# Kernel optimization log

Measured on AMD Instinct MI355X. Metric: run time of the kernel, lower is better.

## Reference

```python
import jax, jax.numpy as jnp
import numpy as np
from math import sqrt

L, H, D, HD, F, V, P = 8, 16, 1024, 64, 4096, 32000, 2048
B, S = 2, 2048
EPS = 1e-5


def _ln(x, g, b):
    m = jnp.mean(x, axis=-1, keepdims=True)
    v = jnp.mean((x - m) ** 2, axis=-1, keepdims=True)
    return (x - m) * jax.lax.rsqrt(v + EPS) * g + b


def setup_inputs() -> dict:
    key = jax.random.key(0)
    ks = jax.random.split(key, 12)
    w = 0.02
    return {
        'input_ids': jax.random.randint(ks[0], (B, S), 0, V),
        'tok_emb': jax.random.normal(ks[1], (V, D), jnp.float32) * w,
        'pos_emb': jax.random.normal(ks[2], (P, D), jnp.float32) * w,
        'emb_g': jnp.ones((D,), jnp.float32),
        'emb_b': jnp.zeros((D,), jnp.float32),
        'ln1_g': jnp.ones((L, D), jnp.float32),
        'ln1_b': jnp.zeros((L, D), jnp.float32),
        'ln2_g': jnp.ones((L, D), jnp.float32),
        'ln2_b': jnp.zeros((L, D), jnp.float32),
        'Wq': jax.random.normal(ks[3], (L, H, D, HD), jnp.float32) * w,
        'bq': jnp.zeros((L, H, HD), jnp.float32),
        'Wk': jax.random.normal(ks[4], (L, H, D, HD), jnp.float32) * w,
        'bk': jnp.zeros((L, H, HD), jnp.float32),
        'Wv': jax.random.normal(ks[5], (L, H, D, HD), jnp.float32) * w,
        'bv': jnp.zeros((L, H, HD), jnp.float32),
        'Wo': jax.random.normal(ks[6], (L, D, D), jnp.float32) * w,
        'bo': jnp.zeros((L, D), jnp.float32),
        'W1': jax.random.normal(ks[7], (L, D, F), jnp.float32) * w,
        'b1': jnp.zeros((L, F), jnp.float32),
        'W2': jax.random.normal(ks[8], (L, F, D), jnp.float32) * w,
        'b2': jnp.zeros((L, D), jnp.float32),
    }


def _encoder(input_ids, tok_emb, pos_emb, emb_g, emb_b, ln1_g, ln1_b, ln2_g,
             ln2_b, Wq, bq, Wk, bk, Wv, bv, Wo, bo, W1, b1, W2, b2):
    seq = input_ids.shape[-1]
    x = tok_emb[input_ids] + pos_emb[:seq][None, :, :]  # [B,S,D]
    x = _ln(x, emb_g, emb_b)  # dropout = identity (eval)

    scale = 1.0 / sqrt(HD)

    def layer(x, p):
        (g1, b1_, g2, b2_, wq, bq_, wk, bk_, wv, bv_, wo, bo_, w1, bb1, w2, bb2) = p
        h = _ln(x, g1, b1_)
        q = jnp.einsum('bsd,hdk->bhsk', h, wq) + bq_[:, None, :]
        k = jnp.einsum('bsd,hdk->bhsk', h, wk) + bk_[:, None, :]
        v = jnp.einsum('bsd,hdk->bhsk', h, wv) + bv_[:, None, :]
        scores = jnp.einsum('bhsk,bhtk->bhst', q, k) * scale
        w = jax.nn.softmax(scores, axis=-1)
        av = jnp.einsum('bhst,bhtk->bhsk', w, v)  # [B,H,S,hd]
        av = jnp.transpose(av, (0, 2, 1, 3)).reshape(x.shape[0], x.shape[1], D)
        x = x + jnp.einsum('bsd,de->bse', av, wo) + bo_
        h2 = _ln(x, g2, b2_)
        f = jax.nn.gelu(jnp.einsum('bsd,df->bsf', h2, w1) + bb1, approximate=False)
        x = x + jnp.einsum('bsf,fd->bsd', f, w2) + bb2
        return x, None

    xs = (ln1_g, ln1_b, ln2_g, ln2_b, Wq, bq, Wk, bk, Wv, bv, Wo, bo, W1, b1, W2, b2)
    x, _ = jax.lax.scan(layer, x, xs)
    return x


def reference(input_ids, tok_emb, pos_emb, emb_g, emb_b, ln1_g, ln1_b, ln2_g,
              ln2_b, Wq, bq, Wk, bk, Wv, bv, Wo, bo, W1, b1, W2, b2):
    return _encoder(input_ids, tok_emb, pos_emb, emb_g, emb_b, ln1_g, ln1_b,
                    ln2_g, ln2_b, Wq, bq, Wk, bk, Wv, bv, Wo, bo, W1, b1, W2, b2)
```

## Files before the change

kernel.cpp:

```cpp
#include <hip/hip_runtime.h>
#include <hip/hip_bf16.h>

#define L_ 8
#define H_ 16
#define D_ 1024
#define HD_ 64
#define F_ 4096
#define B_ 2
#define S_ 2048
#define NTOK (B_*S_)

typedef unsigned short u16;
typedef __bf16 bf16x8 __attribute__((ext_vector_type(8)));
typedef float f32x4 __attribute__((ext_vector_type(4)));

__device__ __forceinline__ u16 f2b(float f){ union{float f; unsigned u;} c; c.f = f; unsigned u = c.u; return (u16)((u + 0x7fffu + ((u>>16)&1u)) >> 16); }
__device__ __forceinline__ u16 f2b_fast(float f){ union{float f; unsigned u;} c; c.f = f; return (u16)((c.u + 0x8000u) >> 16); }
__device__ __forceinline__ float b2f(u16 x){ union{unsigned u; float f;} c; c.u = ((unsigned)x)<<16; return c.f; }

__device__ __forceinline__ void gload16(const u16* g, u16* l){
  __builtin_amdgcn_global_load_lds(
      (const __attribute__((address_space(1))) void*)g,
      (__attribute__((address_space(3))) void*)l,
      16 , 0 , 0 );
}

__device__ __forceinline__ void lds_fence(){
  asm volatile("s_waitcnt lgkmcnt(0)" ::: "memory");
  __builtin_amdgcn_sched_barrier(0);
}

#define WAITV_BAR(n) do { \
  asm volatile("s_waitcnt vmcnt(%0)" :: "i"(n) : "memory"); \
  __builtin_amdgcn_sched_barrier(0); \
  __builtin_amdgcn_s_barrier(); \
} while(0)

__device__ __forceinline__ void blk_reduce2(float& a, float& b, float* sm){
  for (int off=32; off>0; off>>=1){ a += __shfl_down(a,off); b += __shfl_down(b,off); }
  int w = threadIdx.x>>6, ln = threadIdx.x&63;
  if (ln==0){ sm[w]=a; sm[4+w]=b; }
  __syncthreads();
  a = sm[0]+sm[1]+sm[2]+sm[3];
  b = sm[4]+sm[5]+sm[6]+sm[7];
}

__global__ __launch_bounds__(256) void embed_ln(const int* __restrict__ ids,
    const float* __restrict__ tok, const float* __restrict__ pos,
    const float* __restrict__ g, const float* __restrict__ bb,
    float* __restrict__ x)
{
  __shared__ float sm[8];
  int row = blockIdx.x;
  int s   = row % S_;
  int id  = ids[row];
  int d0  = threadIdx.x*4;
  float4 t4 = *(const float4*)(tok + (size_t)id*D_ + d0);
  float4 p4 = *(const float4*)(pos + (size_t)s *D_ + d0);
  float4 v; v.x=t4.x+p4.x; v.y=t4.y+p4.y; v.z=t4.z+p4.z; v.w=t4.w+p4.w;
  float sum = (v.x+v.y)+(v.z+v.w);
  float sq  = v.x*v.x+v.y*v.y+v.z*v.z+v.w*v.w;
  blk_reduce2(sum, sq, sm);
  float mean = sum * (1.0f/D_);
  float var  = sq  * (1.0f/D_) - mean*mean;
  float inv  = rsqrtf(var + 1e-5f);
  float4 g4 = *(const float4*)(g + d0);
  float4 b4 = *(const float4*)(bb + d0);
  float4 o; o.x=(v.x-mean)*inv*g4.x+b4.x; o.y=(v.y-mean)*inv*g4.y+b4.y;
            o.z=(v.z-mean)*inv*g4.z+b4.z; o.w=(v.w-mean)*inv*g4.w+b4.w;
  *(float4*)(x + (size_t)row*D_ + d0) = o;
}

__global__ __launch_bounds__(256) void ln_f32_bf16(const float* __restrict__ x,
    const float* __restrict__ g, const float* __restrict__ bb, u16* __restrict__ out)
{
  __shared__ float sm[8];
  int row = blockIdx.x;
  int d0  = threadIdx.x*4;
  float4 v = *(const float4*)(x + (size_t)row*D_ + d0);
  float sum = (v.x+v.y)+(v.z+v.w);
  float sq  = v.x*v.x+v.y*v.y+v.z*v.z+v.w*v.w;
  blk_reduce2(sum, sq, sm);
  float mean = sum * (1.0f/D_);
  float var  = sq  * (1.0f/D_) - mean*mean;
  float inv  = rsqrtf(var + 1e-5f);
  float4 g4 = *(const float4*)(g + d0);
  float4 b4 = *(const float4*)(bb + d0);
  uint2 w;
  w.x = (unsigned)f2b((v.x-mean)*inv*g4.x+b4.x) | ((unsigned)f2b((v.y-mean)*inv*g4.y+b4.y)<<16);
  w.y = (unsigned)f2b((v.z-mean)*inv*g4.z+b4.z) | ((unsigned)f2b((v.w-mean)*inv*g4.w+b4.w)<<16);
  *(uint2*)(out + (size_t)row*D_ + d0) = w;
}

__global__ __launch_bounds__(256) void transpose_w(const float* __restrict__ src,
    u16* __restrict__ dst, int R, int C)
{
  __shared__ u16 tile[64*64];
  int c0 = blockIdx.x*64, r0 = blockIdx.y*64;
  int t = threadIdx.x;
  #pragma unroll
  for (int i=0;i<2;i++){
    int idx = t + i*256;
    int row = idx>>3, c8 = idx&7;
    const float* p = src + (size_t)(r0+row)*C + c0 + c8*8;
    float4 a = *(const float4*)p;
    float4 b = *(const float4*)(p+4);
    u16 tmp[8];
    tmp[0]=f2b(a.x); tmp[1]=f2b(a.y); tmp[2]=f2b(a.z); tmp[3]=f2b(a.w);
    tmp[4]=f2b(b.x); tmp[5]=f2b(b.y); tmp[6]=f2b(b.z); tmp[7]=f2b(b.w);
    int sw = (row&7) ^ ((row>>3)&7);
    *(uint4*)(&tile[row*64 + ((c8 ^ sw)<<3)]) = *(uint4*)tmp;
  }
  __syncthreads();
  #pragma unroll
  for (int i=0;i<2;i++){
    int idx = t + i*256;
    int oc = idx>>3, tc = idx&7;
    u16 tmp[8];
    #pragma unroll
    for (int j=0;j<8;j++){
      int rr = tc*8 + j;
      int sw = (rr&7) ^ ((rr>>3)&7);
      tmp[j] = tile[rr*64 + ((((oc>>3) ^ sw)<<3) | (oc&7))];
    }
    *(uint4*)(dst + (size_t)(c0+oc)*R + r0 + tc*8) = *(uint4*)tmp;
  }
}

__global__ __launch_bounds__(256) void qkv_repack(const float* __restrict__ Wq,
    const float* __restrict__ Wk, const float* __restrict__ Wv,
    u16* __restrict__ dst, int layer)
{
  __shared__ u16 tile[64*64];
  int z = blockIdx.y; int which = z >> 4, h = z & 15;
  const float* W = (which==0) ? Wq : (which==1) ? Wk : Wv;
  const float* src = W + ((size_t)(layer*H_ + h))*D_*HD_;
  int r0 = blockIdx.x*64;
  int t = threadIdx.x;
  #pragma unroll
  for (int i=0;i<2;i++){
    int idx = t + i*256;
    int row = idx>>3, c8 = idx&7;
    const float* p = src + (size_t)(r0+row)*HD_ + c8*8;
    float4 a = *(const float4*)p;
    float4 b = *(const float4*)(p+4);
    u16 tmp[8];
    tmp[0]=f2b(a.x); tmp[1]=f2b(a.y); tmp[2]=f2b(a.z); tmp[3]=f2b(a.w);
    tmp[4]=f2b(b.x); tmp[5]=f2b(b.y); tmp[6]=f2b(b.z); tmp[7]=f2b(b.w);
    int sw = (row&7) ^ ((row>>3)&7);
    *(uint4*)(&tile[row*64 + ((c8 ^ sw)<<3)]) = *(uint4*)tmp;
  }
  __syncthreads();
  #pragma unroll
  for (int i=0;i<2;i++){
    int idx = t + i*256;
    int oc = idx>>3, tc = idx&7;
    u16 tmp[8];
    #pragma unroll
    for (int j=0;j<8;j++){
      int rr = tc*8 + j;
      int sw = (rr&7) ^ ((rr>>3)&7);
      tmp[j] = tile[rr*64 + ((((oc>>3) ^ sw)<<3) | (oc&7))];
    }
    *(uint4*)(dst + (size_t)(which*1024 + h*64 + oc)*D_ + r0 + tc*8) = *(uint4*)tmp;
  }
}

__global__ __launch_bounds__(256) void v_transpose(const u16* __restrict__ qkv, u16* __restrict__ vT)
{
  __shared__ u16 tile[64*64];
  const int tt = blockIdx.x;
  const int bh = blockIdx.y;
  const int b = bh>>4, h = bh&15;
  const int t = threadIdx.x;
  const u16* src = qkv + (size_t)(b*S_ + tt*64)*3072 + 2048 + h*64;
  #pragma unroll
  for (int i=0;i<2;i++){
    int idx = t + i*256;
    int tl = idx>>3, hc = idx&7;
    uint4 v = *(const uint4*)(src + (size_t)tl*3072 + hc*8);
    int sw = (tl&7) ^ ((tl>>3)&7);
    *(uint4*)(&tile[tl*64 + ((hc ^ sw)<<3)]) = v;
  }
  __syncthreads();
  u16* dst = vT + ((size_t)bh*64)*S_ + tt*64;
  #pragma unroll
  for (int i=0;i<2;i++){
    int idx = t + i*256;
    int hd = idx>>3, tc = idx&7;
    u16 tmp[8];
    #pragma unroll
    for (int j=0;j<8;j++){
      int tk = tc*8 + j;
      int sw = (tk&7) ^ ((tk>>3)&7);
      tmp[j] = tile[tk*64 + ((((hd>>3) ^ sw)<<3) | (hd&7))];
    }
    *(uint4*)(dst + (size_t)hd*S_ + tc*8) = *(uint4*)tmp;
  }
}

__device__ __forceinline__ void epi_store(float v0,float v1,float v2,float v3,
    float* xres, u16* obf, size_t idx, int epi)
{
  if (epi==1){
    float4 t = *(float4*)(xres + idx);
    t.x += v0; t.y += v1; t.z += v2; t.w += v3;
    *(float4*)(xres + idx) = t;
  } else {
    if (epi==2){
      #define GELU_T(v) { float t2=(v)*(v); float u=(v)*fmaf(t2,0.044715f,1.0f); \
                          float e=exp2f(u*-2.3022082f); (v)=(v)*__builtin_amdgcn_rcpf(1.0f+e); }
      GELU_T(v0); GELU_T(v1); GELU_T(v2); GELU_T(v3);
      #undef GELU_T
    }
    uint2 w;
    w.x = (unsigned)f2b_fast(v0) | ((unsigned)f2b_fast(v1) << 16);
    w.y = (unsigned)f2b_fast(v2) | ((unsigned)f2b_fast(v3) << 16);
    *(uint2*)(obf + idx) = w;
  }
}

__global__ __launch_bounds__(256) void gemm_64x128(
    const u16* __restrict__ A, const u16* __restrict__ Bt,
    const float* __restrict__ bias0, float* __restrict__ xres,
    int M, int N, int K)
{
  __shared__ u16 As[64*64];
  __shared__ u16 Bs[128*64];
  const int tid = threadIdx.x;
  const int nbx = gridDim.x;
  const int nwg = nbx * gridDim.y;
  int bid = blockIdx.x + nbx*blockIdx.y;
  int nid = (bid & 7)*(nwg >> 3) + (bid >> 3);
  const int bm = (nid % nbx) * 64;
  const int bn = (nid / nbx) * 128;
  const int wv = tid>>6, ln = tid&63;
  const int wr = wv>>1, wc = wv&1;
  const int l15 = ln&15, lhi = ln>>4;
  const int l8 = ln>>3;
  const int c8s = (ln&7) ^ l8;
  f32x4 acc[2][4];
  const f32x4 zero4 = {0.f,0.f,0.f,0.f};
  #pragma unroll
  for (int i=0;i<2;i++)
    #pragma unroll
    for (int j=0;j<4;j++) acc[i][j] = zero4;

  for (int k0 = 0; k0 < K; k0 += 64) {
    #pragma unroll
    for (int i=0;i<2;i++){
      int row = wv*16 + i*8 + l8;
      gload16(A + (size_t)(bm+row)*K + k0 + c8s*8, &As[(wv*16 + i*8)*64]);
    }
    #pragma unroll
    for (int i=0;i<4;i++){
      int row = wv*32 + i*8 + l8;
      gload16(Bt + (size_t)(bn+row)*K + k0 + c8s*8, &Bs[(wv*32 + i*8)*64]);
    }
    __syncthreads();
    #pragma unroll
    for (int ks=0; ks<2; ks++){
      bf16x8 af[2], bfr[4];
      #pragma unroll
      for (int i=0;i<2;i++){
        int ra = wr*32 + i*16 + l15;
        af[i]  = *(const bf16x8*)(&As[ra*64 + (((ks*4+lhi) ^ (ra&7))<<3)]);
      }
      #pragma unroll
      for (int j=0;j<4;j++){
        int rb = wc*64 + j*16 + l15;
        bfr[j] = *(const bf16x8*)(&Bs[rb*64 + (((ks*4+lhi) ^ (rb&7))<<3)]);
      }
      #pragma unroll
      for (int i=0;i<2;i++)
        #pragma unroll
        for (int j=0;j<4;j++)
          acc[i][j] = __builtin_amdgcn_mfma_f32_16x16x32_bf16(bfr[j], af[i], acc[i][j], 0,0,0);
    }
    __syncthreads();
  }

  #pragma unroll
  for (int j=0;j<4;j++){
    int col0 = bn + wc*64 + j*16 + lhi*4;
    float4 bv4 = *(const float4*)(bias0 + col0);
    #pragma unroll
    for (int i=0;i<2;i++){
      int row = bm + wr*32 + i*16 + l15;
      size_t idx = (size_t)row*N + col0;
      float4 t = *(float4*)(xres + idx);
      t.x += acc[i][j][0] + bv4.x;
      t.y += acc[i][j][1] + bv4.y;
      t.z += acc[i][j][2] + bv4.z;
      t.w += acc[i][j][3] + bv4.w;
      *(float4*)(xres + idx) = t;
    }
  }
}

__global__ __launch_bounds__(512,2) void gemm256(
    const u16* __restrict__ A, const u16* __restrict__ Bt,
    const float* __restrict__ bias0, const float* __restrict__ bias1, const float* __restrict__ bias2,
    float* __restrict__ xres, u16* __restrict__ obf,
    int M, int N, int K, int epi)
{
  __shared__ u16 As[2][256*64];
  __shared__ u16 Bs[2][256*64];
  const int tid = threadIdx.x;
  const int nbx = gridDim.x;
  const int nwg = nbx * gridDim.y;
  int bid = blockIdx.x + nbx*blockIdx.y;
  int nid = (bid & 7)*(nwg >> 3) + (bid >> 3);
  const int bm = (nid % nbx) * 256;
  const int bn = (nid / nbx) * 256;
  const int wv = tid>>6, ln = tid&63;
  const int wm = wv>>2, wn = wv&3;
  const int l15 = ln&15, lhi = ln>>4;
  const int l8 = ln>>3;
  const int c8s = (ln&7) ^ l8;

  f32x4 acc[2][2][4][2];
  const f32x4 zero4 = {0.f,0.f,0.f,0.f};
  #pragma unroll
  for (int a=0;a<2;a++)
    #pragma unroll
    for (int b=0;b<2;b++)
      #pragma unroll
      for (int i=0;i<4;i++)
        #pragma unroll
        for (int j=0;j<2;j++) acc[a][b][i][j] = zero4;

  const u16* aB0 = A  + (size_t)(bm + wv*16 + l8)*K + c8s*8;
  const u16* bB0 = Bt + (size_t)(bn + wv*16 + l8)*K + c8s*8;

  #define ISSUE(c, kt) do {                                                  \
    const u16* aB = aB0 + (size_t)(kt)*64;                                   \
    const u16* bB = bB0 + (size_t)(kt)*64;                                   \
    gload16(aB,                 &As[c][(wv*16      )*64]);                   \
    gload16(aB + (size_t)8*K,   &As[c][(wv*16 +   8)*64]);                   \
    gload16(bB,                 &Bs[c][(wv*16      )*64]);                   \
    gload16(bB + (size_t)8*K,   &Bs[c][(wv*16 +   8)*64]);                   \
    gload16(bB + (size_t)128*K, &Bs[c][(128 + wv*16    )*64]);               \
    gload16(bB + (size_t)136*K, &Bs[c][(128 + wv*16 + 8)*64]);               \
    gload16(aB + (size_t)128*K, &As[c][(128 + wv*16    )*64]);               \
    gload16(aB + (size_t)136*K, &As[c][(128 + wv*16 + 8)*64]);               \
  } while(0)

  #define READ_B(c) do {                                                     \
    _Pragma("unroll")                                                        \
    for (int qc=0;qc<2;qc++)                                                 \
      _Pragma("unroll")                                                      \
      for (int j=0;j<2;j++){                                                 \
        int rb = qc*128 + wn*32 + j*16 + l15;                                \
        _Pragma("unroll")                                                    \
        for (int ks=0;ks<2;ks++)                                             \
          bfr[qc][j][ks] = *(const bf16x8*)(&Bs[c][rb*64 + (((ks*4+lhi) ^ (rb&7))<<3)]); \
      }                                                                      \
  } while(0)

  #define READ_A(c, qr) do {                                                 \
    _Pragma("unroll")                                                        \
    for (int i=0;i<4;i++){                                                   \
      int ra = (qr)*128 + wm*64 + i*16 + l15;                                \
      _Pragma("unroll")                                                      \
      for (int ks=0;ks<2;ks++)                                               \
        af[i][ks] = *(const bf16x8*)(&As[c][ra*64 + (((ks*4+lhi) ^ (ra&7))<<3)]); \
    }                                                                        \
  } while(0)

  #define MFMA_Q(qr) do {                                                    \
    __builtin_amdgcn_s_setprio(1);                                           \
    _Pragma("unroll")                                                        \
    for (int ks=0;ks<2;ks++)                                                 \
      _Pragma("unroll")                                                      \
      for (int i=0;i<4;i++)                                                  \
        _Pragma("unroll")                                                    \
        for (int qc=0;qc<2;qc++)                                             \
          _Pragma("unroll")                                                  \
          for (int j=0;j<2;j++)                                              \
            acc[qr][qc][i][j] = __builtin_amdgcn_mfma_f32_16x16x32_bf16(     \
                bfr[qc][j][ks], af[i][ks], acc[qr][qc][i][j], 0,0,0);        \
    __builtin_amdgcn_s_setprio(0);                                           \
  } while(0)

  const int nt = K >> 6;
  ISSUE(0, 0);
  WAITV_BAR(2);
  for (int t=0; t<nt-1; ++t){
    int c = t&1;
    ISSUE(c^1, t+1);
    bf16x8 bfr[2][2][2], af[4][2];
    READ_B(c);
    READ_A(c, 0);
    MFMA_Q(0);
    WAITV_BAR(8);
    READ_A(c, 1);
    MFMA_Q(1);
    WAITV_BAR(2);
  }
  {
    int c = (nt-1)&1;
    bf16x8 bfr[2][2][2], af[4][2];
    READ_B(c);
    READ_A(c, 0);
    MFMA_Q(0);
    WAITV_BAR(0);
    READ_A(c, 1);
    MFMA_Q(1);
  }
  #undef ISSUE
  #undef READ_B
  #undef READ_A
  #undef MFMA_Q

  #pragma unroll
  for (int qc=0; qc<2; qc++)
    #pragma unroll
    for (int j=0;j<2;j++){
      int col0 = bn + qc*128 + wn*32 + j*16 + lhi*4;
      float4 bv4;
      if (bias1){
        const float* bp = (col0 < 1024) ? (bias0 + col0)
                        : (col0 < 2048) ? (bias1 + col0 - 1024)
                                        : (bias2 + col0 - 2048);
        bv4 = *(const float4*)bp;
      } else {
        bv4 = *(const float4*)(bias0 + col0);
      }
      #pragma unroll
      for (int qr=0; qr<2; qr++)
        #pragma unroll
        for (int i=0;i<4;i++){
          int row = bm + qr*128 + wm*64 + i*16 + l15;
          epi_store(acc[qr][qc][i][j][0]+bv4.x, acc[qr][qc][i][j][1]+bv4.y,
                    acc[qr][qc][i][j][2]+bv4.z, acc[qr][qc][i][j][3]+bv4.w,
                    xres, obf, (size_t)row*N + col0, epi);
        }
    }
}

__global__ __launch_bounds__(256) void attn_fwd(const u16* __restrict__ qkv,
    const u16* __restrict__ vT, u16* __restrict__ att)
{
  __shared__ u16 Ks[2][64*64];
  __shared__ u16 Vs[2][64*64];
  __shared__ u16 Ps[4][2][16*64];
  const int tid = threadIdx.x, wv = tid>>6, ln = tid&63, l15 = ln&15, lhi = ln>>4;
  const int l8 = ln>>3;
  const int cs = (ln&7) ^ l8;
  int bid = blockIdx.x + 16*(blockIdx.y + 16*blockIdx.z);
  int nid = (bid & 7)*64 + (bid >> 3);
  const int qt = nid & 15, h = (nid >> 4) & 15, b = nid >> 8;
  const u16* qg = qkv + (size_t)b*S_*3072 + h*64;
  const u16* kg = qg + 1024;
  const u16* vtg = vT + ((size_t)(b*16 + h)*64)*S_;

  bf16x8 qfA[2], qfB[2];
  {
    const u16* qrA = qg + (size_t)(qt*128 + wv*32 + l15)*3072;
    const u16* qrB = qrA + (size_t)16*3072;
    u16 ta[16], tb[16];
    *(uint4*)(ta)   = *(const uint4*)(qrA + lhi*8);
    *(uint4*)(ta+8) = *(const uint4*)(qrA + 32 + lhi*8);
    *(uint4*)(tb)   = *(const uint4*)(qrB + lhi*8);
    *(uint4*)(tb+8) = *(const uint4*)(qrB + 32 + lhi*8);
    #pragma unroll
    for (int i=0;i<16;i++){ ta[i] = f2b_fast(b2f(ta[i]) * 0.18033688f);
                            tb[i] = f2b_fast(b2f(tb[i]) * 0.18033688f); }
    qfA[0] = *(const bf16x8*)(ta); qfA[1] = *(const bf16x8*)(ta+8);
    qfB[0] = *(const bf16x8*)(tb); qfB[1] = *(const bf16x8*)(tb+8);
  }
  const f32x4 zero4 = {0.f,0.f,0.f,0.f};
  f32x4 oaccA[4], oaccB[4];
  #pragma unroll
  for (int j=0;j<4;j++){ oaccA[j] = zero4; oaccB[j] = zero4; }
  float lsumA = 0.f, lsumB = 0.f;

  const int qsw = (l15&7)<<3;
  u16* PsA = &Ps[wv][0][l15*64];
  u16* PsB = &Ps[wv][1][l15*64];

  #define STAGE_KV(bufi, kti) do {                                            \
    _Pragma("unroll")                                                         \
    for (int i_=0;i_<2;i_++){                                                 \
      int r0_ = wv*8 + i_*32;                                                 \
      int row_ = r0_ + l8;                                                    \
      gload16(kg  + (size_t)((kti)*64+row_)*3072 + cs*8, &Ks[bufi][r0_*64]);  \
      gload16(vtg + (size_t)row_*S_ + (kti)*64 + cs*8,   &Vs[bufi][r0_*64]);  \
    }                                                                         \
  } while(0)

  STAGE_KV(0, 0);
  __syncthreads();
  int buf = 0;

  for (int kt=0; kt<S_/64; kt++){
    if (kt+1 < S_/64) STAGE_KV(buf^1, kt+1);

    f32x4 sA[4], sB[4];
    __builtin_amdgcn_s_setprio(1);
    #pragma unroll
    for (int j=0;j<4;j++){
      sA[j] = zero4; sB[j] = zero4;
      #pragma unroll
      for (int ks=0; ks<2; ks++){
        int kr = j*16 + l15;
        bf16x8 kf = *(const bf16x8*)(&Ks[buf][kr*64 + (((ks*4+lhi) ^ (kr&7))<<3)]);
        sA[j] = __builtin_amdgcn_mfma_f32_16x16x32_bf16(kf, qfA[ks], sA[j], 0,0,0);
        sB[j] = __builtin_amdgcn_mfma_f32_16x16x32_bf16(kf, qfB[ks], sB[j], 0,0,0);
      }
    }
    __builtin_amdgcn_s_setprio(0);

    float partA = 0.f, partB = 0.f;
    #pragma unroll
    for (int j=0;j<4;j++){
      float a0 = exp2f(sA[j][0]), a1 = exp2f(sA[j][1]), a2 = exp2f(sA[j][2]), a3 = exp2f(sA[j][3]);
      float b0 = exp2f(sB[j][0]), b1 = exp2f(sB[j][1]), b2 = exp2f(sB[j][2]), b3 = exp2f(sB[j][3]);
      partA += (a0+a1)+(a2+a3);
      partB += (b0+b1)+(b2+b3);
      unsigned wA0, wA1, wB0, wB1;
      asm("v_cvt_pk_bf16_f32 %0, %1, %2" : "=v"(wA0) : "v"(a0), "v"(a1));
      asm("v_cvt_pk_bf16_f32 %0, %1, %2" : "=v"(wA1) : "v"(a2), "v"(a3));
      asm("v_cvt_pk_bf16_f32 %0, %1, %2" : "=v"(wB0) : "v"(b0), "v"(b1));
      asm("v_cvt_pk_bf16_f32 %0, %1, %2" : "=v"(wB1) : "v"(b2), "v"(b3));
      int e0 = (j*16 + lhi*4) ^ qsw;
      *(unsigned*)(PsA + e0)     = wA0;
      *(unsigned*)(PsA + e0 + 2) = wA1;
      *(unsigned*)(PsB + e0)     = wB0;
      *(unsigned*)(PsB + e0 + 2) = wB1;
    }
    lsumA += partA; lsumB += partB;

    lds_fence();

    bf16x8 pfA[2], pfB[2];
    pfA[0] = *(const bf16x8*)(PsA + ((lhi     ^ (l15&7))<<3));
    pfA[1] = *(const bf16x8*)(PsA + (((4+lhi) ^ (l15&7))<<3));
    pfB[0] = *(const bf16x8*)(PsB + ((lhi     ^ (l15&7))<<3));
    pfB[1] = *(const bf16x8*)(PsB + (((4+lhi) ^ (l15&7))<<3));

    __builtin_amdgcn_s_setprio(1);
    #pragma unroll
    for (int dj=0; dj<4; dj++){
      #pragma unroll
      for (int ks=0; ks<2; ks++){
        int vr = dj*16 + l15;
        bf16x8 vf = *(const bf16x8*)(&Vs[buf][vr*64 + (((ks*4+lhi) ^ (vr&7))<<3)]);
        oaccA[dj] = __builtin_amdgcn_mfma_f32_16x16x32_bf16(pfA[ks], vf, oaccA[dj], 0,0,0);
        oaccB[dj] = __builtin_amdgcn_mfma_f32_16x16x32_bf16(pfB[ks], vf, oaccB[dj], 0,0,0);
      }
    }
    __builtin_amdgcn_s_setprio(0);
    __syncthreads();
    buf ^= 1;
  }
  #undef STAGE_KV

  float totA = lsumA + __shfl_xor(lsumA, 16); totA += __shfl_xor(totA, 32);
  float totB = lsumB + __shfl_xor(lsumB, 16); totB += __shfl_xor(totB, 32);
  float invA[4], invB[4];
  #pragma unroll
  for (int r=0;r<4;r++){
    invA[r] = __builtin_amdgcn_rcpf(__shfl(totA, lhi*4+r));
    invB[r] = __builtin_amdgcn_rcpf(__shfl(totB, lhi*4+r));
  }

  #pragma unroll
  for (int dj=0; dj<4; dj++){
    #pragma unroll
    for (int r=0;r<4;r++){
      int q = lhi*4 + r;
      int tokA = qt*128 + wv*32 + q;
      int tokB = tokA + 16;
      att[(size_t)(b*S_ + tokA)*D_ + h*HD_ + dj*16 + l15] = f2b_fast(oaccA[dj][r] * invA[r]);
      att[(size_t)(b*S_ + tokB)*D_ + h*HD_ + dj*16 + l15] = f2b_fast(oaccB[dj][r] * invB[r]);
    }
  }
}

extern "C" void kernel_launch(void* const* d_in, const int* in_sizes, int n_in,
                              void* d_out, int out_size, void* d_ws, size_t ws_size,
                              hipStream_t stream)
{
  const int*   ids   = (const int*)d_in[0];
  const float* tok   = (const float*)d_in[1];
  const float* pos   = (const float*)d_in[2];
  const float* emb_g = (const float*)d_in[3];
  const float* emb_b = (const float*)d_in[4];
  const float* ln1g  = (const float*)d_in[5];
  const float* ln1b  = (const float*)d_in[6];
  const float* ln2g  = (const float*)d_in[7];
  const float* ln2b  = (const float*)d_in[8];
  const float* Wq = (const float*)d_in[9];
  const float* bq = (const float*)d_in[10];
  const float* Wk = (const float*)d_in[11];
  const float* bk = (const float*)d_in[12];
  const float* Wv = (const float*)d_in[13];
  const float* bv = (const float*)d_in[14];
  const float* Wo = (const float*)d_in[15];
  const float* bo = (const float*)d_in[16];
  const float* W1 = (const float*)d_in[17];
  const float* b1 = (const float*)d_in[18];
  const float* W2 = (const float*)d_in[19];
  const float* b2 = (const float*)d_in[20];

  float* x = (float*)d_out;
  char* ws = (char*)d_ws;
  u16* h     = (u16*)(ws);
  u16* qkvb  = (u16*)(ws + 8388608);
  u16* att   = (u16*)(ws + 33554432);
  u16* fbuf  = (u16*)(ws + 41943040);
  u16* vT    = fbuf;
  u16* wqkvt = (u16*)(ws + 75497472);
  u16* wot   = (u16*)(ws + 81788928);
  u16* w1t   = (u16*)(ws + 83886080);
  u16* w2t   = (u16*)(ws + 92274688);

  embed_ln<<<NTOK, 256, 0, stream>>>(ids, tok, pos, emb_g, emb_b, x);

  for (int l=0; l<L_; l++){
    ln_f32_bf16<<<NTOK, 256, 0, stream>>>(x, ln1g + l*D_, ln1b + l*D_, h);
    qkv_repack<<<dim3(16,48), 256, 0, stream>>>(Wq, Wk, Wv, wqkvt, l);
    gemm256<<<dim3(16,12), 512, 0, stream>>>(h, wqkvt,
        bq + l*1024, bk + l*1024, bv + l*1024,
        nullptr, qkvb, NTOK, 3072, 1024, 0);
    v_transpose<<<dim3(32,32), 256, 0, stream>>>(qkvb, vT);
    attn_fwd<<<dim3(S_/128, H_, B_), 256, 0, stream>>>(qkvb, vT, att);
    transpose_w<<<dim3(16,16), 256, 0, stream>>>(Wo + (size_t)l*D_*D_, wot, D_, D_);
    gemm_64x128<<<dim3(64,8), 256, 0, stream>>>(att, wot,
        bo + l*D_, x, NTOK, 1024, 1024);
    ln_f32_bf16<<<NTOK, 256, 0, stream>>>(x, ln2g + l*D_, ln2b + l*D_, h);
    transpose_w<<<dim3(64,16), 256, 0, stream>>>(W1 + (size_t)l*D_*F_, w1t, D_, F_);
    gemm256<<<dim3(16,16), 512, 0, stream>>>(h, w1t,
        b1 + l*F_, nullptr, nullptr,
        nullptr, fbuf, NTOK, 4096, 1024, 2);
    transpose_w<<<dim3(16,64), 256, 0, stream>>>(W2 + (size_t)l*F_*D_, w2t, F_, D_);
    gemm_64x128<<<dim3(64,8), 256, 0, stream>>>(fbuf, w2t,
        b2 + l*D_, x, NTOK, 1024, 4096);
  }
}
```

Measured before the change: 2.176 ms.

## Use 2 waves per attention block with 64 query rows per wave

The attention kernel now runs with 128 threads (2 waves) instead of 256 (4 waves). Each wave processes 64 query rows as four 16-row groups instead of 32, so every K/V fragment read from LDS feeds four MFMAs rather than two. This halves LDS reads of K/V per unit of compute. The cost is more registers per wave (accumulators and scores quadruple) and fewer waves per block, each of which does more of the K/V staging.

```diff
diff --git a/kernel.cpp b/kernel.cpp
--- a/kernel.cpp
+++ b/kernel.cpp
@@ -439,12 +439,12 @@
     }
 }
 
-__global__ __launch_bounds__(256) void attn_fwd(const u16* __restrict__ qkv,
+__global__ __launch_bounds__(128) void attn_fwd(const u16* __restrict__ qkv,
     const u16* __restrict__ vT, u16* __restrict__ att)
 {
   __shared__ u16 Ks[2][64*64];
   __shared__ u16 Vs[2][64*64];
-  __shared__ u16 Ps[4][2][16*64];
+  __shared__ u16 Ps[2][4][16*64];
   const int tid = threadIdx.x, wv = tid>>6, ln = tid&63, l15 = ln&15, lhi = ln>>4;
   const int l8 = ln>>3;
   const int cs = (ln&7) ^ l8;
@@ -455,35 +455,32 @@
   const u16* kg = qg + 1024;
   const u16* vtg = vT + ((size_t)(b*16 + h)*64)*S_;
 
-  bf16x8 qfA[2], qfB[2];
-  {
-    const u16* qrA = qg + (size_t)(qt*128 + wv*32 + l15)*3072;
-    const u16* qrB = qrA + (size_t)16*3072;
-    u16 ta[16], tb[16];
-    *(uint4*)(ta)   = *(const uint4*)(qrA + lhi*8);
-    *(uint4*)(ta+8) = *(const uint4*)(qrA + 32 + lhi*8);
-    *(uint4*)(tb)   = *(const uint4*)(qrB + lhi*8);
-    *(uint4*)(tb+8) = *(const uint4*)(qrB + 32 + lhi*8);
-    #pragma unroll
-    for (int i=0;i<16;i++){ ta[i] = f2b_fast(b2f(ta[i]) * 0.18033688f);
-                            tb[i] = f2b_fast(b2f(tb[i]) * 0.18033688f); }
-    qfA[0] = *(const bf16x8*)(ta); qfA[1] = *(const bf16x8*)(ta+8);
-    qfB[0] = *(const bf16x8*)(tb); qfB[1] = *(const bf16x8*)(tb+8);
+  bf16x8 qf[4][2];
+  #pragma unroll
+  for (int g=0; g<4; g++){
+    const u16* qr = qg + (size_t)(qt*128 + wv*64 + g*16 + l15)*3072;
+    u16 t16[16];
+    *(uint4*)(t16)   = *(const uint4*)(qr + lhi*8);
+    *(uint4*)(t16+8) = *(const uint4*)(qr + 32 + lhi*8);
+    #pragma unroll
+    for (int i=0;i<16;i++) t16[i] = f2b_fast(b2f(t16[i]) * 0.18033688f);
+    qf[g][0] = *(const bf16x8*)(t16);
+    qf[g][1] = *(const bf16x8*)(t16+8);
   }
   const f32x4 zero4 = {0.f,0.f,0.f,0.f};
-  f32x4 oaccA[4], oaccB[4];
-  #pragma unroll
-  for (int j=0;j<4;j++){ oaccA[j] = zero4; oaccB[j] = zero4; }
-  float lsumA = 0.f, lsumB = 0.f;
+  f32x4 oacc[4][4];
+  #pragma unroll
+  for (int g=0;g<4;g++)
+    #pragma unroll
+    for (int j=0;j<4;j++) oacc[g][j] = zero4;
+  float lsum[4] = {0.f,0.f,0.f,0.f};
 
   const int qsw = (l15&7)<<3;
-  u16* PsA = &Ps[wv][0][l15*64];
-  u16* PsB = &Ps[wv][1][l15*64];
 
   #define STAGE_KV(bufi, kti) do {                                            \
     _Pragma("unroll")                                                         \
-    for (int i_=0;i_<2;i_++){                                                 \
-      int r0_ = wv*8 + i_*32;                                                 \
+    for (int i_=0;i_<4;i_++){                                                 \
+      int r0_ = wv*32 + i_*8;                                                 \
       int row_ = r0_ + l8;                                                    \
       gload16(kg  + (size_t)((kti)*64+row_)*3072 + cs*8, &Ks[bufi][r0_*64]);  \
       gload16(vtg + (size_t)row_*S_ + (kti)*64 + cs*8,   &Vs[bufi][r0_*64]);  \
@@ -497,48 +494,51 @@
   for (int kt=0; kt<S_/64; kt++){
     if (kt+1 < S_/64) STAGE_KV(buf^1, kt+1);
 
-    f32x4 sA[4], sB[4];
+    f32x4 s[4][4];
     __builtin_amdgcn_s_setprio(1);
     #pragma unroll
     for (int j=0;j<4;j++){
-      sA[j] = zero4; sB[j] = zero4;
+      #pragma unroll
+      for (int g=0;g<4;g++) s[g][j] = zero4;
       #pragma unroll
       for (int ks=0; ks<2; ks++){
         int kr = j*16 + l15;
         bf16x8 kf = *(const bf16x8*)(&Ks[buf][kr*64 + (((ks*4+lhi) ^ (kr&7))<<3)]);
-        sA[j] = __builtin_amdgcn_mfma_f32_16x16x32_bf16(kf, qfA[ks], sA[j], 0,0,0);
-        sB[j] = __builtin_amdgcn_mfma_f32_16x16x32_bf16(kf, qfB[ks], sB[j], 0,0,0);
+        #pragma unroll
+        for (int g=0;g<4;g++)
+          s[g][j] = __builtin_amdgcn_mfma_f32_16x16x32_bf16(kf, qf[g][ks], s[g][j], 0,0,0);
       }
     }
     __builtin_amdgcn_s_setprio(0);
 
-    float partA = 0.f, partB = 0.f;
-    #pragma unroll
-    for (int j=0;j<4;j++){
-      float a0 = exp2f(sA[j][0]), a1 = exp2f(sA[j][1]), a2 = exp2f(sA[j][2]), a3 = exp2f(sA[j][3]);
-      float b0 = exp2f(sB[j][0]), b1 = exp2f(sB[j][1]), b2 = exp2f(sB[j][2]), b3 = exp2f(sB[j][3]);
-      partA += (a0+a1)+(a2+a3);
-      partB += (b0+b1)+(b2+b3);
-      unsigned wA0, wA1, wB0, wB1;
-      asm("v_cvt_pk_bf16_f32 %0, %1, %2" : "=v"(wA0) : "v"(a0), "v"(a1));
-      asm("v_cvt_pk_bf16_f32 %0, %1, %2" : "=v"(wA1) : "v"(a2), "v"(a3));
-      asm("v_cvt_pk_bf16_f32 %0, %1, %2" : "=v"(wB0) : "v"(b0), "v"(b1));
-      asm("v_cvt_pk_bf16_f32 %0, %1, %2" : "=v"(wB1) : "v"(b2), "v"(b3));
-      int e0 = (j*16 + lhi*4) ^ qsw;
-      *(unsigned*)(PsA + e0)     = wA0;
-      *(unsigned*)(PsA + e0 + 2) = wA1;
-      *(unsigned*)(PsB + e0)     = wB0;
-      *(unsigned*)(PsB + e0 + 2) = wB1;
-    }
-    lsumA += partA; lsumB += partB;
+    #pragma unroll
+    for (int g=0;g<4;g++){
+      u16* PsG = &Ps[wv][g][l15*64];
+      float part = 0.f;
+      #pragma unroll
+      for (int j=0;j<4;j++){
+        float p0 = exp2f(s[g][j][0]), p1 = exp2f(s[g][j][1]);
+        float p2 = exp2f(s[g][j][2]), p3 = exp2f(s[g][j][3]);
+        part += (p0+p1)+(p2+p3);
+        unsigned w0, w1;
+        asm("v_cvt_pk_bf16_f32 %0, %1, %2" : "=v"(w0) : "v"(p0), "v"(p1));
+        asm("v_cvt_pk_bf16_f32 %0, %1, %2" : "=v"(w1) : "v"(p2), "v"(p3));
+        int e0 = (j*16 + lhi*4) ^ qsw;
+        *(unsigned*)(PsG + e0)     = w0;
+        *(unsigned*)(PsG + e0 + 2) = w1;
+      }
+      lsum[g] += part;
+    }
 
     lds_fence();
 
-    bf16x8 pfA[2], pfB[2];
-    pfA[0] = *(const bf16x8*)(PsA + ((lhi     ^ (l15&7))<<3));
-    pfA[1] = *(const bf16x8*)(PsA + (((4+lhi) ^ (l15&7))<<3));
-    pfB[0] = *(const bf16x8*)(PsB + ((lhi     ^ (l15&7))<<3));
-    pfB[1] = *(const bf16x8*)(PsB + (((4+lhi) ^ (l15&7))<<3));
+    bf16x8 pf[4][2];
+    #pragma unroll
+    for (int g=0;g<4;g++){
+      u16* PsG = &Ps[wv][g][l15*64];
+      pf[g][0] = *(const bf16x8*)(PsG + ((lhi     ^ (l15&7))<<3));
+      pf[g][1] = *(const bf16x8*)(PsG + (((4+lhi) ^ (l15&7))<<3));
+    }
 
     __builtin_amdgcn_s_setprio(1);
     #pragma unroll
@@ -547,8 +547,9 @@
       for (int ks=0; ks<2; ks++){
         int vr = dj*16 + l15;
         bf16x8 vf = *(const bf16x8*)(&Vs[buf][vr*64 + (((ks*4+lhi) ^ (vr&7))<<3)]);
-        oaccA[dj] = __builtin_amdgcn_mfma_f32_16x16x32_bf16(pfA[ks], vf, oaccA[dj], 0,0,0);
-        oaccB[dj] = __builtin_amdgcn_mfma_f32_16x16x32_bf16(pfB[ks], vf, oaccB[dj], 0,0,0);
+        #pragma unroll
+        for (int g=0;g<4;g++)
+          oacc[g][dj] = __builtin_amdgcn_mfma_f32_16x16x32_bf16(pf[g][ks], vf, oacc[g][dj], 0,0,0);
       }
     }
     __builtin_amdgcn_s_setprio(0);
@@ -557,26 +558,25 @@
   }
   #undef STAGE_KV
 
-  float totA = lsumA + __shfl_xor(lsumA, 16); totA += __shfl_xor(totA, 32);
-  float totB = lsumB + __shfl_xor(lsumB, 16); totB += __shfl_xor(totB, 32);
-  float invA[4], invB[4];
-  #pragma unroll
-  for (int r=0;r<4;r++){
-    invA[r] = __builtin_amdgcn_rcpf(__shfl(totA, lhi*4+r));
-    invB[r] = __builtin_amdgcn_rcpf(__shfl(totB, lhi*4+r));
-  }
-
-  #pragma unroll
-  for (int dj=0; dj<4; dj++){
-    #pragma unroll
-    for (int r=0;r<4;r++){
-      int q = lhi*4 + r;
-      int tokA = qt*128 + wv*32 + q;
-      int tokB = tokA + 16;
-      att[(size_t)(b*S_ + tokA)*D_ + h*HD_ + dj*16 + l15] = f2b_fast(oaccA[dj][r] * invA[r]);
-      att[(size_t)(b*S_ + tokB)*D_ + h*HD_ + dj*16 + l15] = f2b_fast(oaccB[dj][r] * invB[r]);
-    }
-  }
+  float inv[4][4];
+  #pragma unroll
+  for (int g=0;g<4;g++){
+    float tot = lsum[g] + __shfl_xor(lsum[g], 16);
+    tot += __shfl_xor(tot, 32);
+    #pragma unroll
+    for (int r=0;r<4;r++) inv[g][r] = __builtin_amdgcn_rcpf(__shfl(tot, lhi*4+r));
+  }
+
+  #pragma unroll
+  for (int g=0;g<4;g++)
+    #pragma unroll
+    for (int dj=0; dj<4; dj++)
+      #pragma unroll
+      for (int r=0;r<4;r++){
+        int q = lhi*4 + r;
+        int token = qt*128 + wv*64 + g*16 + q;
+        att[(size_t)(b*S_ + token)*D_ + h*HD_ + dj*16 + l15] = f2b_fast(oacc[g][dj][r] * inv[g][r]);
+      }
 }
 
 extern "C" void kernel_launch(void* const* d_in, const int* in_sizes, int n_in,
@@ -626,7 +626,7 @@
         bq + l*1024, bk + l*1024, bv + l*1024,
         nullptr, qkvb, NTOK, 3072, 1024, 0);
     v_transpose<<<dim3(32,32), 256, 0, stream>>>(qkvb, vT);
-    attn_fwd<<<dim3(S_/128, H_, B_), 256, 0, stream>>>(qkvb, vT, att);
+    attn_fwd<<<dim3(S_/128, H_, B_), 128, 0, stream>>>(qkvb, vT, att);
     transpose_w<<<dim3(16,16), 256, 0, stream>>>(Wo + (size_t)l*D_*D_, wot, D_, D_);
     gemm_64x128<<<dim3(64,8), 256, 0, stream>>>(att, wot,
         bo + l*D_, x, NTOK, 1024, 1024);
```

After: 2.312 ms. 1.06x slower.
